# Optimization experiments

Hardware: AMD Instinct MI355X
Metric: run time of the kernel (lower is better)

## Reference

```python
import jax, jax.numpy as jnp
from jax import lax
import numpy as np

B, N0 = 4, 4096
NIN, NH, NOUT = 16, 128, 2
DEPTH, K, RADIUS, KNN = 3, 64, 2.0, 3
EPS = 1e-5


def _bn(x, g, b):
    # eval-mode BatchNorm1d with running_mean=0, running_var=1
    return g * x / jnp.sqrt(1.0 + EPS) + b


def _mlp2(h, p):
    # Seq(Lin, ReLU, BN) x 2, as in MLP([d, d, out])
    w1, b1, g1, be1, w2, b2, g2, be2 = p
    h = _bn(jax.nn.relu(h @ w1 + b1), g1, be1)
    return _bn(jax.nn.relu(h @ w2 + b2), g2, be2)


def _fps(pts, m):
    # farthest point sampling, deterministic start at index 0
    n = pts.shape[0]
    def step(carry, _):
        dmin, last = carry
        d = jnp.sum((pts - pts[last]) ** 2, axis=-1)
        dmin = jnp.minimum(dmin, d)
        nxt = jnp.argmax(dmin).astype(jnp.int32)
        return (dmin, nxt), nxt
    _, rest = lax.scan(step, (jnp.full((n,), 1e30, pts.dtype), jnp.int32(0)), None, length=m - 1)
    return jnp.concatenate([jnp.zeros((1,), jnp.int32), rest])


def _sa(xx, pp, m, params):
    # SAModule with PointConv: fps -> radius(K nearest within r) -> gather-MLP-max
    idx = _fps(pp, m)
    q = pp[idx]                                              # [m,3] sampled centers
    d2 = jnp.sum((q[:, None, :] - pp[None, :, :]) ** 2, -1)  # [m,n]
    d2 = jnp.where(d2 <= RADIUS * RADIUS, d2, 1e30)
    neg, nbr = lax.top_k(-d2, K)                             # K nearest inside ball
    valid = neg > -1e29
    h = jnp.concatenate([xx[nbr], pp[nbr] - q[:, None, :]], axis=-1)  # [m,K,C+3]
    h = _mlp2(h, params)
    h = jnp.where(valid[..., None], h, -1e30)
    return jnp.max(h, axis=1), q                             # PointConv max aggr


def _fp(xx, pp, xs, ps, params):
    # FPModule: knn_interpolate (k=3, inverse squared-distance weights) + concat skip + MLP
    d2 = jnp.sum((ps[:, None, :] - pp[None, :, :]) ** 2, -1)  # [n_fine, n_coarse]
    neg, idx = lax.top_k(-d2, KNN)
    w = 1.0 / jnp.maximum(-neg, 1e-16)
    y = jnp.sum(w[..., None] * xx[idx], axis=1) / jnp.sum(w, axis=1, keepdims=True)
    return _mlp2(jnp.concatenate([y, xs], axis=-1), params)


def _forward(x, pos, lin_in_w, lin_in_b,
             sa_w1, sa_b1, sa_g1, sa_be1, sa_w2, sa_b2, sa_g2, sa_be2,
             fp_w1, fp_b1, fp_g1, fp_be1, fp_w2, fp_b2, fp_g2, fp_be2,
             lo_w1, lo_b1, lo_g1, lo_be1, lo_w2, lo_b2, lo_g2, lo_be2):
    xb = jax.nn.relu(x.reshape(B, N0, NIN) @ lin_in_w + lin_in_b)  # lin_in + ReLU
    posb = pos.reshape(B, N0, 3)
    sa = [(xb, posb)]
    n = N0
    for i in range(DEPTH):
        m = n // 2  # ratio = 0.5
        p = (sa_w1[i], sa_b1[i], sa_g1[i], sa_be1[i], sa_w2[i], sa_b2[i], sa_g2[i], sa_be2[i])
        h, q = jax.vmap(lambda a, b: _sa(a, b, m, p))(sa[i][0], sa[i][1])
        sa.append((h, q))
        n = m
    xf, posf = sa[DEPTH]
    for step in range(DEPTH):
        mi = DEPTH - 1 - step
        xs, ps = sa[DEPTH - 1 - step]
        p = (fp_w1[mi], fp_b1[mi], fp_g1[mi], fp_be1[mi], fp_w2[mi], fp_b2[mi], fp_g2[mi], fp_be2[mi])
        xf = jax.vmap(lambda a, b, c, d: _fp(a, b, c, d, p))(xf, posf, xs, ps)
        posf = ps
    out = _mlp2(xf, (lo_w1, lo_b1, lo_g1, lo_be1, lo_w2, lo_b2, lo_g2, lo_be2))
    return out.reshape(B * N0, NOUT)


def setup_inputs() -> dict:
    key = jax.random.key(0)
    ki = iter(jax.random.split(key, 24))
    def nrm(shape, s=0.1):
        return jax.random.normal(next(ki), shape, jnp.float32) * s
    D = NH + 3   # PointConv MLP in-dim
    F = 2 * NH   # FP MLP in-dim (nIn + nSkip)
    return {
        "x": jax.random.normal(next(ki), (B * N0, NIN), jnp.float32),
        "pos": jax.random.uniform(next(ki), (B * N0, 3), jnp.float32) * 16.0,
        "batch": jnp.repeat(jnp.arange(B, dtype=jnp.int32), N0),
        "lin_in_w": nrm((NIN, NH)), "lin_in_b": nrm((NH,)),
        "sa_w1": nrm((DEPTH, D, D)), "sa_b1": nrm((DEPTH, D)),
        "sa_g1": jnp.ones((DEPTH, D)), "sa_be1": jnp.zeros((DEPTH, D)),
        "sa_w2": nrm((DEPTH, D, NH)), "sa_b2": nrm((DEPTH, NH)),
        "sa_g2": jnp.ones((DEPTH, NH)), "sa_be2": jnp.zeros((DEPTH, NH)),
        "fp_w1": nrm((DEPTH, F, F)), "fp_b1": nrm((DEPTH, F)),
        "fp_g1": jnp.ones((DEPTH, F)), "fp_be1": jnp.zeros((DEPTH, F)),
        "fp_w2": nrm((DEPTH, F, NH)), "fp_b2": nrm((DEPTH, NH)),
        "fp_g2": jnp.ones((DEPTH, NH)), "fp_be2": jnp.zeros((DEPTH, NH)),
        "lo_w1": nrm((NH, NH)), "lo_b1": nrm((NH,)),
        "lo_g1": jnp.ones((NH,)), "lo_be1": jnp.zeros((NH,)),
        "lo_w2": nrm((NH, NOUT)), "lo_b2": nrm((NOUT,)),
        "lo_g2": jnp.ones((NOUT,)), "lo_be2": jnp.zeros((NOUT,)),
    }


def reference(x, pos, batch, lin_in_w, lin_in_b,
              sa_w1, sa_b1, sa_g1, sa_be1, sa_w2, sa_b2, sa_g2, sa_be2,
              fp_w1, fp_b1, fp_g1, fp_be1, fp_w2, fp_b2, fp_g2, fp_be2,
              lo_w1, lo_b1, lo_g1, lo_be1, lo_w2, lo_b2, lo_g2, lo_be2):
    return _forward(x, pos, lin_in_w, lin_in_b,
                    sa_w1, sa_b1, sa_g1, sa_be1, sa_w2, sa_b2, sa_g2, sa_be2,
                    fp_w1, fp_b1, fp_g1, fp_be1, fp_w2, fp_b2, fp_g2, fp_be2,
                    lo_w1, lo_b1, lo_g1, lo_be1, lo_w2, lo_b2, lo_g2, lo_be2)
```

## Files before the change

### kernel.cpp

```cpp
#include <hip/hip_runtime.h>
#include <cstddef>


#define EPSF 1e-5f

typedef __attribute__((ext_vector_type(2))) float f32x2;

__device__ __forceinline__ f32x2 f2splat(float s) {
    f32x2 v; v.x = s; v.y = s; return v;
}

__device__ __forceinline__ float d2_rn(float dx, float dy, float dz) {
    return __fadd_rn(__fadd_rn(__fmul_rn(dx, dx), __fmul_rn(dy, dy)), __fmul_rn(dz, dz));
}

template <int CTRL, int RMASK>
__device__ __forceinline__ float dpp_max_f32(float v) {
    int o = __builtin_amdgcn_update_dpp(__float_as_int(v), __float_as_int(v),
                                        CTRL, RMASK, 0xf, false);
    return fmaxf(v, __int_as_float(o));
}

template <int N, int NT>
__device__ void fps_role(const float* __restrict__ pts, float* __restrict__ q,
                         const int m, const int b, char* smem) {
#pragma clang fp contract(off)
    constexpr int PPT = N / NT;
    constexpr int PH = PPT / 2;
    constexpr int NW = NT / 64;
    float* s_px = (float*)smem;
    float* s_py = s_px + N;
    float* s_pz = s_py + N;
    int*   s_qi = (int*)(s_pz + N);
    float2* s_slot = (float2*)(s_qi + N / 2);
    const int t = threadIdx.x;
    const int wave = t >> 6, lane = t & 63;
    const int base = t * PPT;
    const float* P = pts + (size_t)b * N * 3;
    asm volatile("s_setprio 3");
    f32x2 rx[PH], ry[PH], rz[PH], dmin[PH];
#pragma unroll
    for (int j = 0; j < PH; ++j) {
        int i = base + 2 * j;
        float x0 = P[i * 3 + 0], y0 = P[i * 3 + 1], z0 = P[i * 3 + 2];
        float x1 = P[i * 3 + 3], y1 = P[i * 3 + 4], z1 = P[i * 3 + 5];
        rx[j].x = x0; rx[j].y = x1;
        ry[j].x = y0; ry[j].y = y1;
        rz[j].x = z0; rz[j].y = z1;
        dmin[j] = f2splat(1e30f);
        s_px[i] = x0; s_px[i + 1] = x1;
        s_py[i] = y0; s_py[i + 1] = y1;
        s_pz[i] = z0; s_pz[i + 1] = z1;
    }
    float lx = P[0], ly = P[1], lz = P[2];
    if (t == 0) s_qi[0] = 0;

    for (int step = 1; step < m; ++step) {
        float bv = -1.0f; int bj = 0;
        const f32x2 lxv = f2splat(lx), lyv = f2splat(ly), lzv = f2splat(lz);
#pragma unroll
        for (int j = 0; j < PH; ++j) {
            f32x2 dx = rx[j] - lxv;
            f32x2 dy = ry[j] - lyv;
            f32x2 dz = rz[j] - lzv;
            f32x2 d = dx * dx + dy * dy + dz * dz;
            float m0 = fminf(dmin[j].x, d.x);
            float m1 = fminf(dmin[j].y, d.y);
            dmin[j].x = m0; dmin[j].y = m1;
            if (m0 > bv) { bv = m0; bj = 2 * j; }
            if (m1 > bv) { bv = m1; bj = 2 * j + 1; }
        }
        const int bidx = base + bj;

        float v = bv;
        v = dpp_max_f32<0x111, 0xf>(v);
        v = dpp_max_f32<0x112, 0xf>(v);
        v = dpp_max_f32<0x114, 0xf>(v);
        v = dpp_max_f32<0x118, 0xf>(v);
        v = dpp_max_f32<0x142, 0xa>(v);
        v = dpp_max_f32<0x143, 0xc>(v);
        const float mv = __int_as_float(__builtin_amdgcn_readlane(__float_as_int(v), 63));
        unsigned long long mb = __ballot(bv == mv);
        const int wl = __ffsll((long long)mb) - 1;
        const int wbi = __builtin_amdgcn_readlane(bidx, wl);

        const int p = step & 1;
        if (lane == 0) s_slot[p * NW + wave] = make_float2(mv, __int_as_float(wbi));
        __syncthreads();

        float2 sl = s_slot[p * NW + (lane & (NW - 1))];
        float gvt = sl.x;
        gvt = dpp_max_f32<0x111, 0xf>(gvt);
        gvt = dpp_max_f32<0x112, 0xf>(gvt);
        if (NW == 8) gvt = dpp_max_f32<0x114, 0xf>(gvt);
        const float gm = __int_as_float(
            __builtin_amdgcn_readlane(__float_as_int(gvt), NW - 1));
        unsigned long long gb = __ballot((lane < NW) && (sl.x == gm));
        const int gl = __ffsll((long long)gb) - 1;
        const int gi = __builtin_amdgcn_readlane(__float_as_int(sl.y), gl);

        lx = s_px[gi]; ly = s_py[gi]; lz = s_pz[gi];
        if (t == 0) s_qi[step] = gi;
    }
    __syncthreads();
    for (int e = t; e < m; e += NT) {
        int gi = s_qi[e];
        size_t o = ((size_t)b * m + e) * 3;
        q[o] = s_px[gi]; q[o + 1] = s_py[gi]; q[o + 2] = s_pz[gi];
    }
}

__device__ void lin_role(const float* __restrict__ x, const float* __restrict__ w,
                         const float* __restrict__ bias, float* __restrict__ xb,
                         const int blk) {
    const int t = threadIdx.x;
    const int row = blk * 2 + (t >> 7);
    const int col = t & 127;
    float acc = bias[col];
#pragma unroll
    for (int k = 0; k < 16; ++k) acc = fmaf(x[row * 16 + k], w[k * 128 + col], acc);
    xb[row * 128 + col] = fmaxf(acc, 0.0f);
}

template <int CHUNK, int WACT>
__device__ void nbr_role(const float* __restrict__ pts, const float* __restrict__ q,
                         int2* __restrict__ pairs, unsigned* __restrict__ counter,
                         const int n, const int m, const int blk, char* smem) {
    const int w = threadIdx.x >> 6, lane = threadIdx.x & 63;
    if (w >= WACT) return;
    float* D = (float*)smem + w * CHUNK * 64;
    const int c = blk * WACT + w;
    const int b = c / m;
    const float* P = pts + (size_t)b * n * 3;
    const float qx = q[(size_t)c * 3 + 0];
    const float qy = q[(size_t)c * 3 + 1];
    const float qz = q[(size_t)c * 3 + 2];
    for (int s = 0; s < CHUNK; ++s) {
        int i = s * 64 + lane;
        float d2 = d2_rn(P[i * 3] - qx, P[i * 3 + 1] - qy, P[i * 3 + 2] - qz);
        D[i] = (d2 <= 4.0f) ? d2 : 1e30f;
    }
    int my_g = -1;
    int cnt = 0;
    for (int round = 0; round < 64; ++round) {
        float bv = 3e38f;
        int bi = 0x7fffffff;
        for (int s = 0; s < CHUNK; ++s) {
            int i = s * 64 + lane;
            float v = D[i];
            if (v < bv) { bv = v; bi = i; }
        }
#pragma unroll
        for (int off = 32; off >= 1; off >>= 1) {
            float ov = __shfl_xor(bv, off, 64);
            int   oi = __shfl_xor(bi, off, 64);
            if (ov < bv || (ov == bv && oi < bi)) { bv = ov; bi = oi; }
        }
        if (bv > 1e29f) break;
        if (round == lane) my_g = bi;
        if (lane == (bi & 63)) D[bi] = 3e38f;
        ++cnt;
    }
    unsigned base = 0;
    if (lane == 0) base = atomicAdd(counter, (unsigned)cnt);
    base = (unsigned)__shfl((int)base, 0, 64);
    if (lane < cnt) pairs[base + lane] = make_int2(c, my_g);
}

typedef float Row132[132];
__device__ void sa_body(const float* __restrict__ xx, const float* __restrict__ pts,
    const float* __restrict__ q, const int2* __restrict__ pairs,
    const unsigned* __restrict__ vcount,
    const float* __restrict__ w1, const float* __restrict__ b1,
    const float* __restrict__ g1, const float* __restrict__ be1,
    const float* __restrict__ w2, const float* __restrict__ b2,
    const float* __restrict__ g2, const float* __restrict__ be2,
    float* __restrict__ hout, const int lm, const int ln, const int blk, char* smem) {
    Row132* shA = (Row132*)smem;
    Row132* shW = (Row132*)(smem + 33792);
    int* sh_c = (int*)(smem + 50688);
    int* sh_g = sh_c + 64;
    const int t = threadIdx.x;
    const int V = (int)*vcount;
    const int r0 = blk * 64;
    if (r0 >= V) return;
    if (t < 64) {
        int r = r0 + t;
        if (r < V) { int2 p = pairs[r]; sh_c[t] = p.x; sh_g[t] = p.y; }
        else { sh_c[t] = -1; sh_g[t] = 0; }
    }
    __syncthreads();

    for (int e = t; e < 64 * 33; e += 256) {
        int row = e / 33, cid = e - row * 33;
        int c = sh_c[row];
        float4 v = make_float4(0.f, 0.f, 0.f, 0.f);
        if (c >= 0) {
            int g = sh_g[row];
            int b = c >> lm;
            size_t pt = ((size_t)(b << ln) + g);
            if (cid < 32) {
                v = *(const float4*)(xx + (pt << 7) + cid * 4);
            } else {
                const float* P = pts + pt * 3;
                const float* Q = q + (size_t)c * 3;
                v.x = P[0] - Q[0]; v.y = P[1] - Q[1]; v.z = P[2] - Q[2]; v.w = 0.f;
            }
        }
        *(float4*)&shA[row][cid * 4] = v;
    }
    __syncthreads();

    const float invs = 1.0f / sqrtf(1.0f + EPSF);
    const int tr = t >> 4, tc = t & 15;
    const int xrow = t >> 2, xcol = t & 3;
    float acc[32];
#pragma unroll
    for (int i = 0; i < 32; ++i) acc[i] = 0.0f;
    float accx = 0.0f;

    for (int k0 = 0; k0 < 132; k0 += 32) {
        const int kc = (132 - k0 < 32) ? (132 - k0) : 32;
        for (int e = t; e < kc * 132; e += 256) {
            int kk = e / 132, j = e - kk * 132;
            int k = k0 + kk;
            shW[kk][j] = (k < 131 && j < 131) ? w1[k * 131 + j] : 0.0f;
        }
        __syncthreads();
        for (int kk = 0; kk < kc; kk += 4) {
            const int k = k0 + kk;
            const float4 A0 = *(const float4*)&shA[tr     ][k];
            const float4 A1 = *(const float4*)&shA[tr + 16][k];
            const float4 A2 = *(const float4*)&shA[tr + 32][k];
            const float4 A3 = *(const float4*)&shA[tr + 48][k];
            const float4 AX = *(const float4*)&shA[xrow][k];
            const float a0v[4] = {A0.x, A0.y, A0.z, A0.w};
            const float a1v[4] = {A1.x, A1.y, A1.z, A1.w};
            const float a2v[4] = {A2.x, A2.y, A2.z, A2.w};
            const float a3v[4] = {A3.x, A3.y, A3.z, A3.w};
            const float axv[4] = {AX.x, AX.y, AX.z, AX.w};
#pragma unroll
            for (int u = 0; u < 4; ++u) {
                const float4 w0 = *(const float4*)&shW[kk + u][8 * tc];
                const float4 w1v = *(const float4*)&shW[kk + u][8 * tc + 4];
                const float wa[8] = {w0.x, w0.y, w0.z, w0.w, w1v.x, w1v.y, w1v.z, w1v.w};
#pragma unroll
                for (int j = 0; j < 8; ++j) {
                    acc[0 * 8 + j] = fmaf(a0v[u], wa[j], acc[0 * 8 + j]);
                    acc[1 * 8 + j] = fmaf(a1v[u], wa[j], acc[1 * 8 + j]);
                    acc[2 * 8 + j] = fmaf(a2v[u], wa[j], acc[2 * 8 + j]);
                    acc[3 * 8 + j] = fmaf(a3v[u], wa[j], acc[3 * 8 + j]);
                }
                accx = fmaf(axv[u], shW[kk + u][128 + xcol], accx);
            }
        }
        __syncthreads();
    }
#pragma unroll
    for (int i = 0; i < 4; ++i)
#pragma unroll
        for (int j = 0; j < 8; ++j) {
            int col = 8 * tc + j;
            float z = fmaxf(acc[i * 8 + j] + b1[col], 0.0f);
            shA[tr + 16 * i][col] = g1[col] * z * invs + be1[col];
        }
    if (xcol < 3) {
        int col = 128 + xcol;
        float z = fmaxf(accx + b1[col], 0.0f);
        shA[xrow][col] = g1[col] * z * invs + be1[col];
    } else {
        shA[xrow][131] = 0.0f;
    }

#pragma unroll
    for (int i = 0; i < 32; ++i) acc[i] = 0.0f;
    for (int k0 = 0; k0 < 132; k0 += 32) {
        const int kc = (132 - k0 < 32) ? (132 - k0) : 32;
        for (int e = t; e < kc * 132; e += 256) {
            int kk = e / 132, j = e - kk * 132;
            int k = k0 + kk;
            shW[kk][j] = (k < 131 && j < 128) ? w2[k * 128 + j] : 0.0f;
        }
        __syncthreads();
        for (int kk = 0; kk < kc; kk += 4) {
            const int k = k0 + kk;
            const float4 A0 = *(const float4*)&shA[tr     ][k];
            const float4 A1 = *(const float4*)&shA[tr + 16][k];
            const float4 A2 = *(const float4*)&shA[tr + 32][k];
            const float4 A3 = *(const float4*)&shA[tr + 48][k];
            const float a0v[4] = {A0.x, A0.y, A0.z, A0.w};
            const float a1v[4] = {A1.x, A1.y, A1.z, A1.w};
            const float a2v[4] = {A2.x, A2.y, A2.z, A2.w};
            const float a3v[4] = {A3.x, A3.y, A3.z, A3.w};
#pragma unroll
            for (int u = 0; u < 4; ++u) {
                const float4 w0 = *(const float4*)&shW[kk + u][8 * tc];
                const float4 w1v = *(const float4*)&shW[kk + u][8 * tc + 4];
                const float wa[8] = {w0.x, w0.y, w0.z, w0.w, w1v.x, w1v.y, w1v.z, w1v.w};
#pragma unroll
                for (int j = 0; j < 8; ++j) {
                    acc[0 * 8 + j] = fmaf(a0v[u], wa[j], acc[0 * 8 + j]);
                    acc[1 * 8 + j] = fmaf(a1v[u], wa[j], acc[1 * 8 + j]);
                    acc[2 * 8 + j] = fmaf(a2v[u], wa[j], acc[2 * 8 + j]);
                    acc[3 * 8 + j] = fmaf(a3v[u], wa[j], acc[3 * 8 + j]);
                }
            }
        }
        __syncthreads();
    }
#pragma unroll
    for (int i = 0; i < 4; ++i)
#pragma unroll
        for (int j = 0; j < 8; ++j) {
            int col = 8 * tc + j;
            float z = fmaxf(acc[i * 8 + j] + b2[col], 0.0f);
            shA[tr + 16 * i][col] = g2[col] * z * invs + be2[col];
        }
    __syncthreads();

    if (t < 128) {
        const int col = t;
        float run = -1.0f;
        int cur = sh_c[0];
        for (int row = 0; row < 64; ++row) {
            int c = sh_c[row];
            if (c != cur) {
                if (cur >= 0)
                    atomicMax((unsigned*)&hout[((size_t)cur << 7) + col], __float_as_uint(run));
                run = -1.0f; cur = c;
            }
            run = fmaxf(run, shA[row][col]);
        }
        if (cur >= 0)
            atomicMax((unsigned*)&hout[((size_t)cur << 7) + col], __float_as_uint(run));
    }
}

__device__ void knn_role(const float* __restrict__ pf, const float* __restrict__ pc,
                         int* __restrict__ kidx, float* __restrict__ kw,
                         const int nf, const int nc, const int blk) {
    const int tg = blk * 256 + threadIdx.x;
    const int b = tg / nf;
    const float* F = pf + (size_t)tg * 3;
    const float fx = F[0], fy = F[1], fz = F[2];
    const float* C = pc + (size_t)b * nc * 3;
    float b0 = 1e30f, b1 = 1e30f, b2 = 1e30f;
    int i0 = 0, i1 = 0, i2 = 0;
    for (int j = 0; j < nc; ++j) {
        float d2 = d2_rn(C[j * 3] - fx, C[j * 3 + 1] - fy, C[j * 3 + 2] - fz);
        if (d2 < b0)      { b2 = b1; i2 = i1; b1 = b0; i1 = i0; b0 = d2; i0 = j; }
        else if (d2 < b1) { b2 = b1; i2 = i1; b1 = d2; i1 = j; }
        else if (d2 < b2) { b2 = d2; i2 = j; }
    }
    float w0 = 1.0f / fmaxf(b0, 1e-16f);
    float w1 = 1.0f / fmaxf(b1, 1e-16f);
    float w2 = 1.0f / fmaxf(b2, 1e-16f);
    float inv = 1.0f / (w0 + w1 + w2);
    size_t o = (size_t)tg * 3;
    kidx[o] = i0; kidx[o + 1] = i1; kidx[o + 2] = i2;
    kw[o] = w0 * inv; kw[o + 1] = w1 * inv; kw[o + 2] = w2 * inv;
}

__global__ __launch_bounds__(256) void stage_a_kernel(
    const float* __restrict__ pos, float* __restrict__ q1,
    const float* __restrict__ x, const float* __restrict__ lin_w,
    const float* __restrict__ lin_b, float* __restrict__ xb,
    float* __restrict__ hbuf, unsigned* __restrict__ ctrs) {
    __shared__ __align__(16) char smem[57408];
    const int blk = blockIdx.x;
    if (blk < 4) {
        fps_role<4096, 256>(pos, q1, 2048, blk, smem);
    } else if (blk < 4 + 8192) {
        lin_role(x, lin_w, lin_b, xb, blk - 4);
    } else {
        const int i = blk - 8196;
        *(float4*)(hbuf + (size_t)i * 1024 + threadIdx.x * 4) =
            make_float4(0.f, 0.f, 0.f, 0.f);
        if (i == 0 && threadIdx.x < 3) ctrs[threadIdx.x * 16] = 0u;
    }
}

__global__ __launch_bounds__(256) void stage_b_kernel(
    const float* __restrict__ q1, float* __restrict__ q2,
    const float* __restrict__ pos, int2* __restrict__ pairs1,
    unsigned* __restrict__ ctr0,
    int* __restrict__ kidx2, float* __restrict__ kw2) {
    __shared__ __align__(16) char smem[32768];
    const int blk = blockIdx.x;
    if (blk < 4) fps_role<2048, 256>(q1, q2, 1024, blk, smem);
    else if (blk < 4 + 4096)
        nbr_role<64, 2>(pos, q1, pairs1, ctr0, 4096, 2048, blk - 4, smem);
    else
        knn_role(pos, q1, kidx2, kw2, 4096, 2048, blk - 4100);
}

__global__ __launch_bounds__(256) void stage_c_kernel(
    const float* __restrict__ q2, float* __restrict__ q3,
    const float* __restrict__ q1, int2* __restrict__ pairs2,
    unsigned* __restrict__ ctr1,
    const float* __restrict__ xb, const float* __restrict__ pos,
    const int2* __restrict__ pairs1, const unsigned* __restrict__ ctr0,
    const float* __restrict__ w1, const float* __restrict__ b1,
    const float* __restrict__ g1, const float* __restrict__ be1,
    const float* __restrict__ w2, const float* __restrict__ b2,
    const float* __restrict__ g2, const float* __restrict__ be2,
    float* __restrict__ h1, int* __restrict__ kidx1, float* __restrict__ kw1) {
    __shared__ __align__(16) char smem[51200];
    const int blk = blockIdx.x;
    if (blk < 4) fps_role<1024, 256>(q2, q3, 512, blk, smem);
    else if (blk < 4 + 1024)
        nbr_role<32, 4>(q1, q2, pairs2, ctr1, 2048, 1024, blk - 4, smem);
    else if (blk < 4 + 1024 + 8192)
        sa_body(xb, pos, q1, pairs1, ctr0, w1, b1, g1, be1, w2, b2, g2, be2,
                h1, 11, 12, blk - 1028, smem);
    else
        knn_role(q1, q2, kidx1, kw1, 2048, 1024, blk - 9220);
}

__global__ __launch_bounds__(256) void stage_d_kernel(
    const float* __restrict__ q2, const float* __restrict__ q3,
    int2* __restrict__ pairs3, unsigned* __restrict__ ctr2,
    const float* __restrict__ h1, const float* __restrict__ q1,
    const int2* __restrict__ pairs2, const unsigned* __restrict__ ctr1,
    const float* __restrict__ w1, const float* __restrict__ b1,
    const float* __restrict__ g1, const float* __restrict__ be1,
    const float* __restrict__ w2, const float* __restrict__ b2,
    const float* __restrict__ g2, const float* __restrict__ be2,
    float* __restrict__ h2, int* __restrict__ kidx0, float* __restrict__ kw0) {
    __shared__ __align__(16) char smem[51200];
    const int blk = blockIdx.x;
    if (blk < 512) nbr_role<16, 4>(q2, q3, pairs3, ctr2, 1024, 512, blk, smem);
    else if (blk < 512 + 16) knn_role(q2, q3, kidx0, kw0, 1024, 512, blk - 512);
    else
        sa_body(h1, q1, q2, pairs2, ctr1, w1, b1, g1, be1, w2, b2, g2, be2,
                h2, 10, 11, blk - 528, smem);
}

__global__ __launch_bounds__(256) void sa_fused_kernel(
    const float* xx, const float* pts, const float* q, const int2* pairs,
    const unsigned* vcount,
    const float* w1, const float* b1, const float* g1, const float* be1,
    const float* w2, const float* b2, const float* g2, const float* be2,
    float* hout, int lm, int ln) {
    __shared__ __align__(16) char smem[51200];
    sa_body(xx, pts, q, pairs, vcount, w1, b1, g1, be1, w2, b2, g2, be2,
            hout, lm, ln, blockIdx.x, smem);
}

__global__ __launch_bounds__(256) void fp_fused_kernel(
    const float* __restrict__ xc, const float* __restrict__ xs,
    const int* __restrict__ kidx, const float* __restrict__ kw,
    const float* __restrict__ w1, const float* __restrict__ b1,
    const float* __restrict__ g1, const float* __restrict__ be1,
    const float* __restrict__ w2, const float* __restrict__ b2,
    const float* __restrict__ g2, const float* __restrict__ be2,
    float* __restrict__ out, int lnf) {
    __shared__ __align__(16) float shA[32][260];
    __shared__ __align__(16) float shW[16][256];
    const int t = threadIdx.x;
    const int r0 = blockIdx.x * 32;
    const float invs = 1.0f / sqrtf(1.0f + EPSF);

    for (int e = t; e < 32 * 64; e += 256) {
        int r = e >> 6, cid = e & 63;
        int fr = r0 + r;
        float4 v;
        if (cid < 32) {
            int b = fr >> lnf;
            size_t o = (size_t)fr * 3;
            int i0 = kidx[o], i1 = kidx[o + 1], i2 = kidx[o + 2];
            float u0 = kw[o], u1 = kw[o + 1], u2 = kw[o + 2];
            const float* X = xc + (((size_t)b << lnf) >> 1) * 128;
            const float4 A0 = *(const float4*)(X + (size_t)i0 * 128 + cid * 4);
            const float4 A1 = *(const float4*)(X + (size_t)i1 * 128 + cid * 4);
            const float4 A2 = *(const float4*)(X + (size_t)i2 * 128 + cid * 4);
            v.x = u0 * A0.x + u1 * A1.x + u2 * A2.x;
            v.y = u0 * A0.y + u1 * A1.y + u2 * A2.y;
            v.z = u0 * A0.z + u1 * A1.z + u2 * A2.z;
            v.w = u0 * A0.w + u1 * A1.w + u2 * A2.w;
        } else {
            v = *(const float4*)(xs + (size_t)fr * 128 + (cid - 32) * 4);
        }
        *(float4*)&shA[r][cid * 4] = v;
    }
    __syncthreads();

    const int tr = t >> 5, tc = t & 31;
    float acc[32];
#pragma unroll
    for (int i = 0; i < 32; ++i) acc[i] = 0.0f;
    for (int k0 = 0; k0 < 256; k0 += 16) {
        for (int e = t; e < 16 * 64; e += 256) {
            int kk = e >> 6, cid = e & 63;
            *(float4*)&shW[kk][cid * 4] =
                *(const float4*)(w1 + (size_t)(k0 + kk) * 256 + cid * 4);
        }
        __syncthreads();
        for (int kk = 0; kk < 16; kk += 4) {
            const int k = k0 + kk;
            const float4 A0 = *(const float4*)&shA[tr     ][k];
            const float4 A1 = *(const float4*)&shA[tr +  8][k];
            const float4 A2 = *(const float4*)&shA[tr + 16][k];
            const float4 A3 = *(const float4*)&shA[tr + 24][k];
            const float a0v[4] = {A0.x, A0.y, A0.z, A0.w};
            const float a1v[4] = {A1.x, A1.y, A1.z, A1.w};
            const float a2v[4] = {A2.x, A2.y, A2.z, A2.w};
            const float a3v[4] = {A3.x, A3.y, A3.z, A3.w};
#pragma unroll
            for (int u = 0; u < 4; ++u) {
                const float4 w0v = *(const float4*)&shW[kk + u][8 * tc];
                const float4 w1v = *(const float4*)&shW[kk + u][8 * tc + 4];
                const float wa[8] = {w0v.x, w0v.y, w0v.z, w0v.w, w1v.x, w1v.y, w1v.z, w1v.w};
#pragma unroll
                for (int j = 0; j < 8; ++j) {
                    acc[0 * 8 + j] = fmaf(a0v[u], wa[j], acc[0 * 8 + j]);
                    acc[1 * 8 + j] = fmaf(a1v[u], wa[j], acc[1 * 8 + j]);
                    acc[2 * 8 + j] = fmaf(a2v[u], wa[j], acc[2 * 8 + j]);
                    acc[3 * 8 + j] = fmaf(a3v[u], wa[j], acc[3 * 8 + j]);
                }
            }
        }
        __syncthreads();
    }
#pragma unroll
    for (int i = 0; i < 4; ++i)
#pragma unroll
        for (int j = 0; j < 8; ++j) {
            int col = 8 * tc + j;
            float z = fmaxf(acc[i * 8 + j] + b1[col], 0.0f);
            shA[tr + 8 * i][col] = g1[col] * z * invs + be1[col];
        }
    __syncthreads();

    const int tr2 = t >> 4, tc2 = t & 15;
    float acc2[16];
#pragma unroll
    for (int i = 0; i < 16; ++i) acc2[i] = 0.0f;
    for (int k0 = 0; k0 < 256; k0 += 16) {
        for (int e = t; e < 16 * 32; e += 256) {
            int kk = e >> 5, cid = e & 31;
            *(float4*)&shW[kk][cid * 4] =
                *(const float4*)(w2 + (size_t)(k0 + kk) * 128 + cid * 4);
        }
        __syncthreads();
        for (int kk = 0; kk < 16; kk += 4) {
            const int k = k0 + kk;
            const float4 A0 = *(const float4*)&shA[tr2     ][k];
            const float4 A1 = *(const float4*)&shA[tr2 + 16][k];
            const float a0v[4] = {A0.x, A0.y, A0.z, A0.w};
            const float a1v[4] = {A1.x, A1.y, A1.z, A1.w};
#pragma unroll
            for (int u = 0; u < 4; ++u) {
                const float4 w0v = *(const float4*)&shW[kk + u][8 * tc2];
                const float4 w1v = *(const float4*)&shW[kk + u][8 * tc2 + 4];
                const float wa[8] = {w0v.x, w0v.y, w0v.z, w0v.w, w1v.x, w1v.y, w1v.z, w1v.w};
#pragma unroll
                for (int j = 0; j < 8; ++j) {
                    acc2[0 * 8 + j] = fmaf(a0v[u], wa[j], acc2[0 * 8 + j]);
                    acc2[1 * 8 + j] = fmaf(a1v[u], wa[j], acc2[1 * 8 + j]);
                }
            }
        }
        __syncthreads();
    }
#pragma unroll
    for (int i = 0; i < 2; ++i)
#pragma unroll
        for (int j = 0; j < 8; ++j) {
            int col = 8 * tc2 + j;
            int fr = r0 + tr2 + 16 * i;
            float z = fmaxf(acc2[i * 8 + j] + b2[col], 0.0f);
            out[(size_t)fr * 128 + col] = g2[col] * z * invs + be2[col];
        }
}

__global__ __launch_bounds__(256) void lo_fused_kernel(
    const float* __restrict__ in,
    const float* __restrict__ w1, const float* __restrict__ b1,
    const float* __restrict__ g1, const float* __restrict__ be1,
    const float* __restrict__ w2, const float* __restrict__ b2,
    const float* __restrict__ g2, const float* __restrict__ be2,
    float* __restrict__ out) {
    __shared__ __align__(16) float shA[32][132];
    __shared__ __align__(16) float shW[16][128];
    const int t = threadIdx.x;
    const int r0 = blockIdx.x * 32;
    const float invs = 1.0f / sqrtf(1.0f + EPSF);

    for (int e = t; e < 32 * 32; e += 256) {
        int r = e >> 5, cid = e & 31;
        *(float4*)&shA[r][cid * 4] =
            *(const float4*)(in + (size_t)(r0 + r) * 128 + cid * 4);
    }
    __syncthreads();

    const int tr = t >> 4, tc = t & 15;
    float acc[16];
#pragma unroll
    for (int i = 0; i < 16; ++i) acc[i] = 0.0f;
    for (int k0 = 0; k0 < 128; k0 += 16) {
        for (int e = t; e < 16 * 32; e += 256) {
            int kk = e >> 5, cid = e & 31;
            *(float4*)&shW[kk][cid * 4] =
                *(const float4*)(w1 + (size_t)(k0 + kk) * 128 + cid * 4);
        }
        __syncthreads();
        for (int kk = 0; kk < 16; ++kk) {
            const int k = k0 + kk;
            float a0 = shA[2 * tr + 0][k], a1 = shA[2 * tr + 1][k];
            const float4 w0v = *(const float4*)&shW[kk][8 * tc];
            const float4 w1v = *(const float4*)&shW[kk][8 * tc + 4];
            const float wa[8] = {w0v.x, w0v.y, w0v.z, w0v.w, w1v.x, w1v.y, w1v.z, w1v.w};
#pragma unroll
            for (int j = 0; j < 8; ++j) {
                acc[0 * 8 + j] = fmaf(a0, wa[j], acc[0 * 8 + j]);
                acc[1 * 8 + j] = fmaf(a1, wa[j], acc[1 * 8 + j]);
            }
        }
        __syncthreads();
    }
#pragma unroll
    for (int i = 0; i < 2; ++i)
#pragma unroll
        for (int j = 0; j < 8; ++j) {
            int col = 8 * tc + j;
            float z = fmaxf(acc[i * 8 + j] + b1[col], 0.0f);
            shA[2 * tr + i][col] = g1[col] * z * invs + be1[col];
        }
    __syncthreads();

    if (t < 64) {
        const int row = t >> 1, col = t & 1;
        float a = b2[col];
        for (int k = 0; k < 128; ++k)
            a = fmaf(shA[row][k], w2[k * 2 + col], a);
        a = fmaxf(a, 0.0f);
        out[(size_t)(r0 + row) * 2 + col] = g2[col] * a * invs + be2[col];
    }
}

extern "C" void kernel_launch(void* const* d_in, const int* in_sizes, int n_in,
                              void* d_out, int out_size, void* d_ws, size_t ws_size,
                              hipStream_t stream) {
    const float* x      = (const float*)d_in[0];
    const float* pos    = (const float*)d_in[1];
    const float* lin_w  = (const float*)d_in[3];
    const float* lin_b  = (const float*)d_in[4];
    const float* sa_w1  = (const float*)d_in[5];
    const float* sa_b1  = (const float*)d_in[6];
    const float* sa_g1  = (const float*)d_in[7];
    const float* sa_be1 = (const float*)d_in[8];
    const float* sa_w2  = (const float*)d_in[9];
    const float* sa_b2  = (const float*)d_in[10];
    const float* sa_g2  = (const float*)d_in[11];
    const float* sa_be2 = (const float*)d_in[12];
    const float* fp_w1  = (const float*)d_in[13];
    const float* fp_b1  = (const float*)d_in[14];
    const float* fp_g1  = (const float*)d_in[15];
    const float* fp_be1 = (const float*)d_in[16];
    const float* fp_w2  = (const float*)d_in[17];
    const float* fp_b2  = (const float*)d_in[18];
    const float* fp_g2  = (const float*)d_in[19];
    const float* fp_be2 = (const float*)d_in[20];
    const float* lo_w1  = (const float*)d_in[21];
    const float* lo_b1  = (const float*)d_in[22];
    const float* lo_g1  = (const float*)d_in[23];
    const float* lo_be1 = (const float*)d_in[24];
    const float* lo_w2  = (const float*)d_in[25];
    const float* lo_b2  = (const float*)d_in[26];
    const float* lo_g2  = (const float*)d_in[27];
    const float* lo_be2 = (const float*)d_in[28];

    float* ws = (float*)d_ws;
    size_t off = 0;
    auto alloc = [&](size_t n) { float* p = ws + off; off += n; return p; };
    float* xb    = alloc(4 * 4096 * 128);
    float* q1    = alloc(4 * 2048 * 3);
    float* q2    = alloc(4 * 1024 * 3);
    float* q3    = alloc(4 * 512 * 3);
    float* h1    = alloc(4 * 2048 * 128);
    float* h2    = alloc(4 * 1024 * 128);
    float* h3    = alloc(4 * 512 * 128);
    int2* pairs1 = (int2*)alloc(4 * 2048 * 64 * 2);
    int2* pairs2 = (int2*)alloc(4 * 1024 * 64 * 2);
    int2* pairs3 = (int2*)alloc(4 * 512 * 64 * 2);
    unsigned* ctrs = (unsigned*)alloc(64);
    int* kidx0   = (int*)alloc(4 * 1024 * 3);
    float* kw0   = alloc(4 * 1024 * 3);
    int* kidx1   = (int*)alloc(4 * 2048 * 3);
    float* kw1   = alloc(4 * 2048 * 3);
    int* kidx2   = (int*)alloc(4 * 4096 * 3);
    float* kw2   = alloc(4 * 4096 * 3);
    float* xfA   = alloc(4 * 4096 * 128);
    float* xfB   = alloc(4 * 4096 * 128);
    if (ws_size < off * sizeof(float)) return;

    stage_a_kernel<<<4 + 8192 + 1792, 256, 0, stream>>>(
        pos, q1, x, lin_w, lin_b, xb, h1, ctrs);

    stage_b_kernel<<<4 + 4096 + 64, 256, 0, stream>>>(
        q1, q2, pos, pairs1, ctrs + 0, kidx2, kw2);

    stage_c_kernel<<<4 + 1024 + 8192 + 32, 256, 0, stream>>>(
        q2, q3, q1, pairs2, ctrs + 16,
        xb, pos, pairs1, ctrs + 0,
        sa_w1, sa_b1, sa_g1, sa_be1, sa_w2, sa_b2, sa_g2, sa_be2, h1,
        kidx1, kw1);

    stage_d_kernel<<<512 + 16 + 4096, 256, 0, stream>>>(
        q2, q3, pairs3, ctrs + 32,
        h1, q1, pairs2, ctrs + 16,
        sa_w1 + 131 * 131, sa_b1 + 131, sa_g1 + 131, sa_be1 + 131,
        sa_w2 + 131 * 128, sa_b2 + 128, sa_g2 + 128, sa_be2 + 128, h2,
        kidx0, kw0);

    sa_fused_kernel<<<2048, 256, 0, stream>>>(h2, q2, q3, pairs3, ctrs + 32,
        sa_w1 + 2 * 131 * 131, sa_b1 + 2 * 131, sa_g1 + 2 * 131, sa_be1 + 2 * 131,
        sa_w2 + 2 * 131 * 128, sa_b2 + 2 * 128, sa_g2 + 2 * 128, sa_be2 + 2 * 128,
        h3, 9, 10);

    fp_fused_kernel<<<4 * 1024 / 32, 256, 0, stream>>>(h3, h2, kidx0, kw0,
        fp_w1 + 2 * 256 * 256, fp_b1 + 2 * 256, fp_g1 + 2 * 256, fp_be1 + 2 * 256,
        fp_w2 + 2 * 256 * 128, fp_b2 + 2 * 128, fp_g2 + 2 * 128, fp_be2 + 2 * 128,
        xfA, 10);

    fp_fused_kernel<<<4 * 2048 / 32, 256, 0, stream>>>(xfA, h1, kidx1, kw1,
        fp_w1 + 256 * 256, fp_b1 + 256, fp_g1 + 256, fp_be1 + 256,
        fp_w2 + 256 * 128, fp_b2 + 128, fp_g2 + 128, fp_be2 + 128,
        xfB, 11);

    fp_fused_kernel<<<4 * 4096 / 32, 256, 0, stream>>>(xfB, xb, kidx2, kw2,
        fp_w1, fp_b1, fp_g1, fp_be1, fp_w2, fp_b2, fp_g2, fp_be2,
        xfA, 12);

    lo_fused_kernel<<<16384 / 32, 256, 0, stream>>>(xfA,
        lo_w1, lo_b1, lo_g1, lo_be1, lo_w2, lo_b2, lo_g2, lo_be2,
        (float*)d_out);
}
```

Before: 3.295 ms.

## Pre-pad SA weights once and read them directly from global memory in SA MLP

Adds a prologue in stage_a that pads the SA layer weights into aligned 132-wide buffers. The SA MLP kernels then read weights straight from global memory (L1/L2 cached) instead of staging them through shared memory in chunks. This drops the per-chunk staging loops and barriers and shrinks the shared-memory footprint, which may allow more resident blocks. The cost is more global or cache traffic inside the inner FMA loop, and possible latency stalls on the weight loads.

Result: faster. 3.108 ms (-5.7%).

```diff
diff --git a/kernel.cpp b/kernel.cpp
--- a/kernel.cpp
+++ b/kernel.cpp
@@ -171,14 +171,13 @@
 __device__ void sa_body(const float* __restrict__ xx, const float* __restrict__ pts,
     const float* __restrict__ q, const int2* __restrict__ pairs,
     const unsigned* __restrict__ vcount,
-    const float* __restrict__ w1, const float* __restrict__ b1,
+    const float* __restrict__ wp1, const float* __restrict__ b1,
     const float* __restrict__ g1, const float* __restrict__ be1,
-    const float* __restrict__ w2, const float* __restrict__ b2,
+    const float* __restrict__ wp2, const float* __restrict__ b2,
     const float* __restrict__ g2, const float* __restrict__ be2,
     float* __restrict__ hout, const int lm, const int ln, const int blk, char* smem) {
     Row132* shA = (Row132*)smem;
-    Row132* shW = (Row132*)(smem + 33792);
-    int* sh_c = (int*)(smem + 50688);
+    int* sh_c = (int*)(smem + 33792);
     int* sh_g = sh_c + 64;
     const int t = threadIdx.x;
     const int V = (int)*vcount;
@@ -219,43 +218,35 @@
     for (int i = 0; i < 32; ++i) acc[i] = 0.0f;
     float accx = 0.0f;
 
-    for (int k0 = 0; k0 < 132; k0 += 32) {
-        const int kc = (132 - k0 < 32) ? (132 - k0) : 32;
-        for (int e = t; e < kc * 132; e += 256) {
-            int kk = e / 132, j = e - kk * 132;
-            int k = k0 + kk;
-            shW[kk][j] = (k < 131 && j < 131) ? w1[k * 131 + j] : 0.0f;
-        }
-        __syncthreads();
-        for (int kk = 0; kk < kc; kk += 4) {
-            const int k = k0 + kk;
-            const float4 A0 = *(const float4*)&shA[tr     ][k];
-            const float4 A1 = *(const float4*)&shA[tr + 16][k];
-            const float4 A2 = *(const float4*)&shA[tr + 32][k];
-            const float4 A3 = *(const float4*)&shA[tr + 48][k];
-            const float4 AX = *(const float4*)&shA[xrow][k];
-            const float a0v[4] = {A0.x, A0.y, A0.z, A0.w};
-            const float a1v[4] = {A1.x, A1.y, A1.z, A1.w};
-            const float a2v[4] = {A2.x, A2.y, A2.z, A2.w};
-            const float a3v[4] = {A3.x, A3.y, A3.z, A3.w};
-            const float axv[4] = {AX.x, AX.y, AX.z, AX.w};
-#pragma unroll
-            for (int u = 0; u < 4; ++u) {
-                const float4 w0 = *(const float4*)&shW[kk + u][8 * tc];
-                const float4 w1v = *(const float4*)&shW[kk + u][8 * tc + 4];
-                const float wa[8] = {w0.x, w0.y, w0.z, w0.w, w1v.x, w1v.y, w1v.z, w1v.w};
-#pragma unroll
-                for (int j = 0; j < 8; ++j) {
-                    acc[0 * 8 + j] = fmaf(a0v[u], wa[j], acc[0 * 8 + j]);
-                    acc[1 * 8 + j] = fmaf(a1v[u], wa[j], acc[1 * 8 + j]);
-                    acc[2 * 8 + j] = fmaf(a2v[u], wa[j], acc[2 * 8 + j]);
-                    acc[3 * 8 + j] = fmaf(a3v[u], wa[j], acc[3 * 8 + j]);
-                }
-                accx = fmaf(axv[u], shW[kk + u][128 + xcol], accx);
+    for (int k = 0; k < 132; k += 4) {
+        const float4 A0 = *(const float4*)&shA[tr     ][k];
+        const float4 A1 = *(const float4*)&shA[tr + 16][k];
+        const float4 A2 = *(const float4*)&shA[tr + 32][k];
+        const float4 A3 = *(const float4*)&shA[tr + 48][k];
+        const float4 AX = *(const float4*)&shA[xrow][k];
+        const float a0v[4] = {A0.x, A0.y, A0.z, A0.w};
+        const float a1v[4] = {A1.x, A1.y, A1.z, A1.w};
+        const float a2v[4] = {A2.x, A2.y, A2.z, A2.w};
+        const float a3v[4] = {A3.x, A3.y, A3.z, A3.w};
+        const float axv[4] = {AX.x, AX.y, AX.z, AX.w};
+#pragma unroll
+        for (int u = 0; u < 4; ++u) {
+            const float* wr = wp1 + (size_t)(k + u) * 132;
+            const float4 w0 = *(const float4*)(wr + 8 * tc);
+            const float4 w1v = *(const float4*)(wr + 8 * tc + 4);
+            const float wx = wr[128 + xcol];
+            const float wa[8] = {w0.x, w0.y, w0.z, w0.w, w1v.x, w1v.y, w1v.z, w1v.w};
+#pragma unroll
+            for (int j = 0; j < 8; ++j) {
+                acc[0 * 8 + j] = fmaf(a0v[u], wa[j], acc[0 * 8 + j]);
+                acc[1 * 8 + j] = fmaf(a1v[u], wa[j], acc[1 * 8 + j]);
+                acc[2 * 8 + j] = fmaf(a2v[u], wa[j], acc[2 * 8 + j]);
+                acc[3 * 8 + j] = fmaf(a3v[u], wa[j], acc[3 * 8 + j]);
             }
-        }
-        __syncthreads();
-    }
+            accx = fmaf(axv[u], wx, accx);
+        }
+    }
+    __syncthreads();
 #pragma unroll
     for (int i = 0; i < 4; ++i)
 #pragma unroll
@@ -271,43 +262,35 @@
     } else {
         shA[xrow][131] = 0.0f;
     }
+    __syncthreads();
 
 #pragma unroll
     for (int i = 0; i < 32; ++i) acc[i] = 0.0f;
-    for (int k0 = 0; k0 < 132; k0 += 32) {
-        const int kc = (132 - k0 < 32) ? (132 - k0) : 32;
-        for (int e = t; e < kc * 132; e += 256) {
-            int kk = e / 132, j = e - kk * 132;
-            int k = k0 + kk;
-            shW[kk][j] = (k < 131 && j < 128) ? w2[k * 128 + j] : 0.0f;
-        }
-        __syncthreads();
-        for (int kk = 0; kk < kc; kk += 4) {
-            const int k = k0 + kk;
-            const float4 A0 = *(const float4*)&shA[tr     ][k];
-            const float4 A1 = *(const float4*)&shA[tr + 16][k];
-            const float4 A2 = *(const float4*)&shA[tr + 32][k];
-            const float4 A3 = *(const float4*)&shA[tr + 48][k];
-            const float a0v[4] = {A0.x, A0.y, A0.z, A0.w};
-            const float a1v[4] = {A1.x, A1.y, A1.z, A1.w};
-            const float a2v[4] = {A2.x, A2.y, A2.z, A2.w};
-            const float a3v[4] = {A3.x, A3.y, A3.z, A3.w};
-#pragma unroll
-            for (int u = 0; u < 4; ++u) {
-                const float4 w0 = *(const float4*)&shW[kk + u][8 * tc];
-                const float4 w1v = *(const float4*)&shW[kk + u][8 * tc + 4];
-                const float wa[8] = {w0.x, w0.y, w0.z, w0.w, w1v.x, w1v.y, w1v.z, w1v.w};
-#pragma unroll
-                for (int j = 0; j < 8; ++j) {
-                    acc[0 * 8 + j] = fmaf(a0v[u], wa[j], acc[0 * 8 + j]);
-                    acc[1 * 8 + j] = fmaf(a1v[u], wa[j], acc[1 * 8 + j]);
-                    acc[2 * 8 + j] = fmaf(a2v[u], wa[j], acc[2 * 8 + j]);
-                    acc[3 * 8 + j] = fmaf(a3v[u], wa[j], acc[3 * 8 + j]);
-                }
+    for (int k = 0; k < 132; k += 4) {
+        const float4 A0 = *(const float4*)&shA[tr     ][k];
+        const float4 A1 = *(const float4*)&shA[tr + 16][k];
+        const float4 A2 = *(const float4*)&shA[tr + 32][k];
+        const float4 A3 = *(const float4*)&shA[tr + 48][k];
+        const float a0v[4] = {A0.x, A0.y, A0.z, A0.w};
+        const float a1v[4] = {A1.x, A1.y, A1.z, A1.w};
+        const float a2v[4] = {A2.x, A2.y, A2.z, A2.w};
+        const float a3v[4] = {A3.x, A3.y, A3.z, A3.w};
+#pragma unroll
+        for (int u = 0; u < 4; ++u) {
+            const float* wr = wp2 + (size_t)(k + u) * 128;
+            const float4 w0 = *(const float4*)(wr + 8 * tc);
+            const float4 w1v = *(const float4*)(wr + 8 * tc + 4);
+            const float wa[8] = {w0.x, w0.y, w0.z, w0.w, w1v.x, w1v.y, w1v.z, w1v.w};
+#pragma unroll
+            for (int j = 0; j < 8; ++j) {
+                acc[0 * 8 + j] = fmaf(a0v[u], wa[j], acc[0 * 8 + j]);
+                acc[1 * 8 + j] = fmaf(a1v[u], wa[j], acc[1 * 8 + j]);
+                acc[2 * 8 + j] = fmaf(a2v[u], wa[j], acc[2 * 8 + j]);
+                acc[3 * 8 + j] = fmaf(a3v[u], wa[j], acc[3 * 8 + j]);
             }
         }
-        __syncthreads();
-    }
+    }
+    __syncthreads();
 #pragma unroll
     for (int i = 0; i < 4; ++i)
 #pragma unroll
@@ -365,18 +348,38 @@
     const float* __restrict__ pos, float* __restrict__ q1,
     const float* __restrict__ x, const float* __restrict__ lin_w,
     const float* __restrict__ lin_b, float* __restrict__ xb,
-    float* __restrict__ hbuf, unsigned* __restrict__ ctrs) {
+    float* __restrict__ hbuf, unsigned* __restrict__ ctrs,
+    const float* __restrict__ sa_w1, const float* __restrict__ sa_w2,
+    float* __restrict__ wp1, float* __restrict__ wp2) {
     __shared__ __align__(16) char smem[57408];
     const int blk = blockIdx.x;
     if (blk < 4) {
         fps_role<4096, 256>(pos, q1, 2048, blk, smem);
     } else if (blk < 4 + 8192) {
         lin_role(x, lin_w, lin_b, xb, blk - 4);
-    } else {
+    } else if (blk < 4 + 8192 + 1792) {
         const int i = blk - 8196;
         *(float4*)(hbuf + (size_t)i * 1024 + threadIdx.x * 4) =
             make_float4(0.f, 0.f, 0.f, 0.f);
         if (i == 0 && threadIdx.x < 3) ctrs[threadIdx.x * 16] = 0u;
+    } else {
+        const int f = (blk - 9988) * 256 + threadIdx.x;
+        if (f < 52272) {
+            int col = f % 132; int r = f / 132;
+            int k = r % 132; int lvl = r / 132;
+            float v = 0.0f;
+            if (k < 131 && col < 131)
+                v = sa_w1[(size_t)lvl * 131 * 131 + k * 131 + col];
+            wp1[f] = v;
+        } else if (f < 52272 + 50688) {
+            int f2 = f - 52272;
+            int col = f2 & 127; int r = f2 >> 7;
+            int k = r % 132; int lvl = r / 132;
+            float v = 0.0f;
+            if (k < 131)
+                v = sa_w2[(size_t)lvl * 131 * 128 + k * 128 + col];
+            wp2[f2] = v;
+        }
     }
 }
 
@@ -400,18 +403,18 @@
     unsigned* __restrict__ ctr1,
     const float* __restrict__ xb, const float* __restrict__ pos,
     const int2* __restrict__ pairs1, const unsigned* __restrict__ ctr0,
-    const float* __restrict__ w1, const float* __restrict__ b1,
+    const float* __restrict__ wp1, const float* __restrict__ b1,
     const float* __restrict__ g1, const float* __restrict__ be1,
-    const float* __restrict__ w2, const float* __restrict__ b2,
+    const float* __restrict__ wp2, const float* __restrict__ b2,
     const float* __restrict__ g2, const float* __restrict__ be2,
     float* __restrict__ h1, int* __restrict__ kidx1, float* __restrict__ kw1) {
-    __shared__ __align__(16) char smem[51200];
+    __shared__ __align__(16) char smem[34304];
     const int blk = blockIdx.x;
     if (blk < 4) fps_role<1024, 256>(q2, q3, 512, blk, smem);
     else if (blk < 4 + 1024)
         nbr_role<32, 4>(q1, q2, pairs2, ctr1, 2048, 1024, blk - 4, smem);
     else if (blk < 4 + 1024 + 8192)
-        sa_body(xb, pos, q1, pairs1, ctr0, w1, b1, g1, be1, w2, b2, g2, be2,
+        sa_body(xb, pos, q1, pairs1, ctr0, wp1, b1, g1, be1, wp2, b2, g2, be2,
                 h1, 11, 12, blk - 1028, smem);
     else
         knn_role(q1, q2, kidx1, kw1, 2048, 1024, blk - 9220);
@@ -422,28 +425,28 @@
     int2* __restrict__ pairs3, unsigned* __restrict__ ctr2,
     const float* __restrict__ h1, const float* __restrict__ q1,
     const int2* __restrict__ pairs2, const unsigned* __restrict__ ctr1,
-    const float* __restrict__ w1, const float* __restrict__ b1,
+    const float* __restrict__ wp1, const float* __restrict__ b1,
     const float* __restrict__ g1, const float* __restrict__ be1,
-    const float* __restrict__ w2, const float* __restrict__ b2,
+    const float* __restrict__ wp2, const float* __restrict__ b2,
     const float* __restrict__ g2, const float* __restrict__ be2,
     float* __restrict__ h2, int* __restrict__ kidx0, float* __restrict__ kw0) {
-    __shared__ __align__(16) char smem[51200];
+    __shared__ __align__(16) char smem[34304];
     const int blk = blockIdx.x;
     if (blk < 512) nbr_role<16, 4>(q2, q3, pairs3, ctr2, 1024, 512, blk, smem);
     else if (blk < 512 + 16) knn_role(q2, q3, kidx0, kw0, 1024, 512, blk - 512);
     else
-        sa_body(h1, q1, q2, pairs2, ctr1, w1, b1, g1, be1, w2, b2, g2, be2,
+        sa_body(h1, q1, q2, pairs2, ctr1, wp1, b1, g1, be1, wp2, b2, g2, be2,
                 h2, 10, 11, blk - 528, smem);
 }
 
 __global__ __launch_bounds__(256) void sa_fused_kernel(
     const float* xx, const float* pts, const float* q, const int2* pairs,
     const unsigned* vcount,
-    const float* w1, const float* b1, const float* g1, const float* be1,
-    const float* w2, const float* b2, const float* g2, const float* be2,
+    const float* wp1, const float* b1, const float* g1, const float* be1,
+    const float* wp2, const float* b2, const float* g2, const float* be2,
     float* hout, int lm, int ln) {
-    __shared__ __align__(16) char smem[51200];
-    sa_body(xx, pts, q, pairs, vcount, w1, b1, g1, be1, w2, b2, g2, be2,
+    __shared__ __align__(16) char smem[34304];
+    sa_body(xx, pts, q, pairs, vcount, wp1, b1, g1, be1, wp2, b2, g2, be2,
             hout, lm, ln, blockIdx.x, smem);
 }
 
@@ -693,10 +696,12 @@
     float* kw2   = alloc(4 * 4096 * 3);
     float* xfA   = alloc(4 * 4096 * 128);
     float* xfB   = alloc(4 * 4096 * 128);
+    float* wp1   = alloc(3 * 132 * 132);
+    float* wp2   = alloc(3 * 132 * 128);
     if (ws_size < off * sizeof(float)) return;
 
-    stage_a_kernel<<<4 + 8192 + 1792, 256, 0, stream>>>(
-        pos, q1, x, lin_w, lin_b, xb, h1, ctrs);
+    stage_a_kernel<<<4 + 8192 + 1792 + 403, 256, 0, stream>>>(
+        pos, q1, x, lin_w, lin_b, xb, h1, ctrs, sa_w1, sa_w2, wp1, wp2);
 
     stage_b_kernel<<<4 + 4096 + 64, 256, 0, stream>>>(
         q1, q2, pos, pairs1, ctrs + 0, kidx2, kw2);
@@ -704,19 +709,19 @@
     stage_c_kernel<<<4 + 1024 + 8192 + 32, 256, 0, stream>>>(
         q2, q3, q1, pairs2, ctrs + 16,
         xb, pos, pairs1, ctrs + 0,
-        sa_w1, sa_b1, sa_g1, sa_be1, sa_w2, sa_b2, sa_g2, sa_be2, h1,
+        wp1, sa_b1, sa_g1, sa_be1, wp2, sa_b2, sa_g2, sa_be2, h1,
         kidx1, kw1);
 
     stage_d_kernel<<<512 + 16 + 4096, 256, 0, stream>>>(
         q2, q3, pairs3, ctrs + 32,
         h1, q1, pairs2, ctrs + 16,
-        sa_w1 + 131 * 131, sa_b1 + 131, sa_g1 + 131, sa_be1 + 131,
-        sa_w2 + 131 * 128, sa_b2 + 128, sa_g2 + 128, sa_be2 + 128, h2,
+        wp1 + 132 * 132, sa_b1 + 131, sa_g1 + 131, sa_be1 + 131,
+        wp2 + 132 * 128, sa_b2 + 128, sa_g2 + 128, sa_be2 + 128, h2,
         kidx0, kw0);
 
     sa_fused_kernel<<<2048, 256, 0, stream>>>(h2, q2, q3, pairs3, ctrs + 32,
-        sa_w1 + 2 * 131 * 131, sa_b1 + 2 * 131, sa_g1 + 2 * 131, sa_be1 + 2 * 131,
-        sa_w2 + 2 * 131 * 128, sa_b2 + 2 * 128, sa_g2 + 2 * 128, sa_be2 + 2 * 128,
+        wp1 + 2 * 132 * 132, sa_b1 + 2 * 131, sa_g1 + 2 * 131, sa_be1 + 2 * 131,
+        wp2 + 2 * 132 * 128, sa_b2 + 2 * 128, sa_g2 + 2 * 128, sa_be2 + 2 * 128,
         h3, 9, 10);
 
     fp_fused_kernel<<<4 * 1024 / 32, 256, 0, stream>>>(h3, h2, kidx0, kw0,
```
